# Kernel tuning notes

Hardware: AMD Instinct MI355X
Metric: run time of the kernel (lower is better)

Reference implementation:

```python
import jax, jax.numpy as jnp
import numpy as np


def _ln(x, g, b, eps=1e-5):
    m = x.mean(-1, keepdims=True)
    v = ((x - m) ** 2).mean(-1, keepdims=True)
    return (x - m) / jnp.sqrt(v + eps) * g + b


def _conv(x, w, b, stride, pad, groups):
    # x: NCHW, w: OIHW (I = in_ch/groups)
    out = jax.lax.conv_general_dilated(
        x, w, (stride, stride), [(pad, pad), (pad, pad)],
        dimension_numbers=('NCHW', 'OIHW', 'NCHW'), feature_group_count=groups)
    return out + b[None, :, None, None]


def _gelu(x):
    return jax.nn.gelu(x, approximate=False)  # torch nn.GELU (exact erf)


def _forward(x, H, W, lpu_w, lpu_b, n1_g, n1_b, conv2d_w, conv2d_b, cn_g, cn_b,
             q_w, sr1_w, sr1_b, an1_g, an1_b, sr2_w, sr2_b, an2_g, an2_b,
             kv1_w, kv2_w, proj_w, proj_b, n2_g, n2_b,
             fc1_w, fc1_b, dw_w, dw_b, fc2_w, fc2_b):
    B, N, C = x.shape
    cd = C // 4          # conv_part_dim = 64
    ad = C - cd          # attn_part_dim = 192
    nh = 8
    hg = nh // 2         # heads per group
    hd = ad // nh        # head_dim = 24
    scale = hd ** -0.5
    # ---- LPU: depthwise 3x3 conv residual ----
    xi = x.transpose(0, 2, 1).reshape(B, C, H, W)
    xi = _conv(xi, lpu_w, lpu_b, 1, 1, C) + xi
    x = xi.reshape(B, C, N).transpose(0, 2, 1)
    # ---- Attention branch (pre-LN) ----
    y = _ln(x, n1_g, n1_b)
    cp, ap = y[..., :cd], y[..., cd:]
    # conv part: dense 3x3 conv (sr_ratio==8 -> kernel 3, pad 1), then LN+GELU in NLC
    cp = cp.reshape(B, H, W, cd).transpose(0, 3, 1, 2)
    cp = _conv(cp, conv2d_w, conv2d_b, 1, 1, 1).reshape(B, cd, N).transpose(0, 2, 1)
    cp = _gelu(_ln(cp, cn_g, cn_b))
    # attn part: dual spatial-reduction KV paths
    q = (ap @ q_w.T).reshape(B, N, nh, hd).transpose(0, 2, 1, 3)  # [B,nh,N,hd]
    x_ = ap.transpose(0, 2, 1).reshape(B, ad, H, W)
    x1 = _conv(x_, sr1_w, sr1_b, 8, 0, ad).reshape(B, ad, -1).transpose(0, 2, 1)  # [B,(H/8)(W/8),ad]
    x1 = _gelu(_ln(x1, an1_g, an1_b))
    x2 = _conv(x_, sr2_w, sr2_b, 4, 0, ad).reshape(B, ad, -1).transpose(0, 2, 1)  # [B,(H/4)(W/4),ad]
    x2 = _gelu(_ln(x2, an2_g, an2_b))
    kv1 = (x1 @ kv1_w.T).reshape(B, -1, 2, hg, hd).transpose(2, 0, 3, 1, 4)  # [2,B,hg,M1,hd]
    kv2 = (x2 @ kv2_w.T).reshape(B, -1, 2, hg, hd).transpose(2, 0, 3, 1, 4)

    def attn(qh, k, v):
        a = jax.nn.softmax(jnp.einsum('bhnd,bhmd->bhnm', qh, k) * scale, axis=-1)
        o = jnp.einsum('bhnm,bhmd->bhnd', a, v)
        return o.transpose(0, 2, 1, 3).reshape(B, N, -1)

    o1 = attn(q[:, :hg], kv1[0], kv1[1])
    o2 = attn(q[:, hg:], kv2[0], kv2[1])
    y = jnp.concatenate([o1, o2, cp], axis=-1) @ proj_w.T + proj_b
    x = x + y
    # ---- MLP with depthwise conv ----
    z = _ln(x, n2_g, n2_b) @ fc1_w.T + fc1_b
    hidc = z.shape[-1]
    z = z.transpose(0, 2, 1).reshape(B, hidc, H, W)
    z = _conv(z, dw_w, dw_b, 1, 1, hidc).reshape(B, hidc, N).transpose(0, 2, 1)
    z = _gelu(z) @ fc2_w.T + fc2_b
    return x + z


def setup_inputs() -> dict:
    key = jax.random.key(0)
    ks = jax.random.split(key, 16)
    B, H, W, C = 16, 56, 56, 256
    N = H * W
    cd, ad = C // 4, C * 3 // 4
    hid = 4 * C
    f = lambda i, shape, s=0.02: jax.random.normal(ks[i], shape, jnp.float32) * s
    return dict(
        x=jax.random.normal(ks[0], (B, N, C), jnp.float32),
        H=H, W=W,
        lpu_w=f(1, (C, 1, 3, 3), 0.1), lpu_b=jnp.zeros((C,), jnp.float32),
        n1_g=jnp.ones((C,), jnp.float32), n1_b=jnp.zeros((C,), jnp.float32),
        conv2d_w=f(2, (cd, cd, 3, 3), 0.05), conv2d_b=jnp.zeros((cd,), jnp.float32),
        cn_g=jnp.ones((cd,), jnp.float32), cn_b=jnp.zeros((cd,), jnp.float32),
        q_w=f(3, (ad, ad)),
        sr1_w=f(4, (ad, 1, 8, 8), 0.1), sr1_b=jnp.zeros((ad,), jnp.float32),
        an1_g=jnp.ones((ad,), jnp.float32), an1_b=jnp.zeros((ad,), jnp.float32),
        sr2_w=f(5, (ad, 1, 4, 4), 0.1), sr2_b=jnp.zeros((ad,), jnp.float32),
        an2_g=jnp.ones((ad,), jnp.float32), an2_b=jnp.zeros((ad,), jnp.float32),
        kv1_w=f(6, (ad, ad)), kv2_w=f(7, (ad, ad)),
        proj_w=f(8, (C, C)), proj_b=jnp.zeros((C,), jnp.float32),
        n2_g=jnp.ones((C,), jnp.float32), n2_b=jnp.zeros((C,), jnp.float32),
        fc1_w=f(9, (hid, C)), fc1_b=jnp.zeros((hid,), jnp.float32),
        dw_w=f(10, (hid, 1, 3, 3), 0.1), dw_b=jnp.zeros((hid,), jnp.float32),
        fc2_w=f(11, (C, hid)), fc2_b=jnp.zeros((C,), jnp.float32),
    )


def reference(x, H, W, lpu_w, lpu_b, n1_g, n1_b, conv2d_w, conv2d_b, cn_g, cn_b,
              q_w, sr1_w, sr1_b, an1_g, an1_b, sr2_w, sr2_b, an2_g, an2_b,
              kv1_w, kv2_w, proj_w, proj_b, n2_g, n2_b,
              fc1_w, fc1_b, dw_w, dw_b, fc2_w, fc2_b):
    return _forward(x, H, W, lpu_w, lpu_b, n1_g, n1_b, conv2d_w, conv2d_b, cn_g, cn_b,
                    q_w, sr1_w, sr1_b, an1_g, an1_b, sr2_w, sr2_b, an2_g, an2_b,
                    kv1_w, kv2_w, proj_w, proj_b, n2_g, n2_b,
                    fc1_w, fc1_b, dw_w, dw_b, fc2_w, fc2_b)
```

## Files before the change

kernel.cpp:

```cpp
#include <hip/hip_runtime.h>
#include <math.h>

#define BB   16
#define HH   56
#define WW   56
#define NN   (HH*WW)
#define CC   256
#define CD   64
#define AD   192
#define NH   8
#define HG   4
#define HD   24
#define HID  1024
#define M1   49
#define M2   196
#define BNR  (BB*NN)

typedef __attribute__((ext_vector_type(8))) short s8v;
typedef __attribute__((ext_vector_type(4))) short s4v;
typedef __attribute__((ext_vector_type(4))) float f4v;
typedef __attribute__((ext_vector_type(8))) _Float16 h8v;
typedef __attribute__((ext_vector_type(2))) _Float16 h2v;

__device__ __forceinline__ float gelu_f(float x) {
    float u = x * (1.0f + 0.044715f * x * x);
    float t = __expf(-1.5957691216f * u);
    return x * __builtin_amdgcn_rcpf(1.0f + t);
}
__device__ __forceinline__ ushort f2bf(float f) {
    union { float f; uint32_t u; } c; c.f = f;
    uint32_t u = c.u;
    return (ushort)((u + 0x7fffu + ((u >> 16) & 1u)) >> 16);
}
__device__ __forceinline__ float bf2f(ushort u) {
    union { uint32_t u; float f; } c; c.u = ((uint32_t)u) << 16;
    return c.f;
}
__device__ __forceinline__ ushort f2h(float f) {
    union { _Float16 h; ushort u; } c; c.h = (_Float16)f;
    return c.u;
}
__device__ __forceinline__ void load_lds16(const void* gsrc, void* ldst) {
    __builtin_amdgcn_global_load_lds(
        (const __attribute__((address_space(1))) void*)gsrc,
        (__attribute__((address_space(3))) void*)ldst, 16, 0, 0);
}
__device__ __forceinline__ int xcd_swz(int bid, int nwg) {
    int q = nwg >> 3, r = nwg & 7;
    int x = bid & 7, i = bid >> 3;
    return (x < r ? x * (q + 1) : r * (q + 1) + (x - r) * q) + i;
}

__global__ __launch_bounds__(256) void wprep_kernel(
        const float* __restrict__ qw, const float* __restrict__ k1,
        const float* __restrict__ k2, const float* __restrict__ pw,
        const float* __restrict__ f1, const float* __restrict__ f2,
        const float* __restrict__ cw, const float* __restrict__ lw,
        const float* __restrict__ dw,
        ushort* __restrict__ wq, ushort* __restrict__ wkv1,
        ushort* __restrict__ wkv2, ushort* __restrict__ wpr,
        ushort* __restrict__ wf1, ushort* __restrict__ wf2,
        ushort* __restrict__ wcp, float* __restrict__ lpwt,
        ushort* __restrict__ dwwth) {
    int i = blockIdx.x * 256 + threadIdx.x;
    if (i < 36864) { wq[i] = f2bf(qw[i]); return; } i -= 36864;
    if (i < 36864) { wkv1[i] = f2bf(k1[i]); return; } i -= 36864;
    if (i < 36864) { wkv2[i] = f2bf(k2[i]); return; } i -= 36864;
    if (i < 65536) { wpr[i] = f2bf(pw[i]); return; } i -= 65536;
    if (i < 262144) { wf1[i] = f2bf(f1[i]); return; } i -= 262144;
    if (i < 262144) { wf2[i] = f2h(f2[i]); return; } i -= 262144;
    if (i < 36864) {
        int co = i / 576, k = i - co * 576;
        int tap = k >> 6, ci = k & 63;
        wcp[i] = f2bf(cw[co * 576 + ci * 9 + tap]);
        return;
    } i -= 36864;
    if (i < 2304) { int c = i / 9, t = i - c * 9; lpwt[t * CC + c] = lw[i]; return; } i -= 2304;
    if (i < 9216) { int c = i / 9, t = i - c * 9; dwwth[t * HID + c] = f2h(dw[i]); }
}

__global__ __launch_bounds__(256) void lpu_kernel(const float* __restrict__ x,
        const float* __restrict__ wt, const float* __restrict__ bias,
        const float* __restrict__ n1g, const float* __restrict__ n1b,
        ushort* __restrict__ xbuf, ushort* __restrict__ ybuf) {
    int tid = threadIdx.x;
    int lane = tid & 63, wv = tid >> 6;
    int c = lane * 4;
    int grp = xcd_swz(blockIdx.x, NN / 16) * 4 + wv;
    int n0 = grp * 4;
    int h = n0 / WW, x0 = n0 - h * WW;
    int b = blockIdx.y;
    const float* xb = x + (size_t)b * NN * CC + c;
    float4 wreg[9];
#pragma unroll
    for (int t = 0; t < 9; ++t) wreg[t] = *(const float4*)(wt + t * CC + c);
    float4 bz = *(const float4*)(bias + c);
    float4 acc[4] = {bz, bz, bz, bz};
#pragma unroll
    for (int cx = 0; cx < 6; ++cx) {
        int wx = x0 + cx - 1;
        if ((unsigned)wx >= (unsigned)WW) continue;
#pragma unroll
        for (int ky = 0; ky < 3; ++ky) {
            int hy = h + ky - 1;
            if ((unsigned)hy >= (unsigned)HH) continue;
            float4 xv = *(const float4*)(xb + (size_t)(hy * WW + wx) * CC);
#pragma unroll
            for (int xo = 0; xo < 4; ++xo) {
                int kx = cx - xo;
                if (kx < 0 || kx > 2) continue;
                float4 wv4 = wreg[ky * 3 + kx];
                acc[xo].x = fmaf(xv.x, wv4.x, acc[xo].x);
                acc[xo].y = fmaf(xv.y, wv4.y, acc[xo].y);
                acc[xo].z = fmaf(xv.z, wv4.z, acc[xo].z);
                acc[xo].w = fmaf(xv.w, wv4.w, acc[xo].w);
            }
        }
    }
    float4 gv = *(const float4*)(n1g + c);
    float4 bv = *(const float4*)(n1b + c);
#pragma unroll
    for (int xo = 0; xo < 4; ++xo) {
        size_t o = ((size_t)b * NN + n0 + xo) * CC + c;
        float4 rv = *(const float4*)(x + o);
        float4 a = acc[xo];
        a.x += rv.x; a.y += rv.y; a.z += rv.z; a.w += rv.w;
        s4v xv4;
        xv4.x = (short)f2bf(a.x);
        xv4.y = (short)f2bf(a.y);
        xv4.z = (short)f2bf(a.z);
        xv4.w = (short)f2bf(a.w);
        *(s4v*)(xbuf + o) = xv4;
        float s = a.x + a.y + a.z + a.w;
        float sq = a.x * a.x + a.y * a.y + a.z * a.z + a.w * a.w;
#pragma unroll
        for (int off = 32; off >= 1; off >>= 1) {
            s += __shfl_xor(s, off, 64);
            sq += __shfl_xor(sq, off, 64);
        }
        float mean = s * (1.0f / 256.0f);
        float var = sq * (1.0f / 256.0f) - mean * mean;
        float rstd = rsqrtf(var + 1e-5f);
        s4v ov;
        ov.x = (short)f2bf((a.x - mean) * rstd * gv.x + bv.x);
        ov.y = (short)f2bf((a.y - mean) * rstd * gv.y + bv.y);
        ov.z = (short)f2bf((a.z - mean) * rstd * gv.z + bv.z);
        ov.w = (short)f2bf((a.w - mean) * rstd * gv.w + bv.w);
        *(s4v*)(ybuf + o) = ov;
    }
}

__device__ __forceinline__ void cpgemm_body(
        const ushort* __restrict__ y, const ushort* __restrict__ wt,
        const float* __restrict__ cb, const float* __restrict__ cng,
        const float* __restrict__ cnb, ushort* __restrict__ cat,
        ushort* As , ushort* Ws , int tile) {
    int tid = threadIdx.x;
    int wid = tid >> 6, lane = tid & 63;
    int rt = xcd_swz(tile, BNR / 128) * 128;
    int r0 = tid >> 2, c0 = tid & 3;
    int r1 = r0 + 64;
    int tok0 = rt + r0, tok1 = rt + r1;
    int b0 = tok0 / NN, n0 = tok0 - b0 * NN, h0 = n0 / WW, w0 = n0 - h0 * WW;
    int b1 = tok1 / NN, n1 = tok1 - b1 * NN, h1 = n1 / WW, w1 = n1 - h1 * WW;
    const ushort* Wp = wt + (size_t)r0 * 576 + c0 * 8;
    int aw0 = (c0 ^ (r0 & 3)) << 3;
    f4v acc[2][4];
#pragma unroll
    for (int m = 0; m < 2; ++m)
#pragma unroll
        for (int n = 0; n < 4; ++n) acc[m][n] = (f4v)0.f;
    int lr = lane & 15, g4 = lane >> 4;
    int swz = (g4 ^ (lr & 3)) << 3;
    for (int kt = 0; kt < 576; kt += 32) {
        int tap = kt >> 6, ci0 = kt & 63;
        int t3 = tap / 3, dy = t3 - 1, dx = (tap - t3 * 3) - 1;
        s8v a0 = (s8v)0, a1 = (s8v)0;
        int hy0 = h0 + dy, wx0 = w0 + dx;
        if ((unsigned)hy0 < (unsigned)HH && (unsigned)wx0 < (unsigned)WW)
            a0 = *(const s8v*)(y + ((size_t)b0 * NN + hy0 * WW + wx0) * CC + ci0 + c0 * 8);
        int hy1 = h1 + dy, wx1 = w1 + dx;
        if ((unsigned)hy1 < (unsigned)HH && (unsigned)wx1 < (unsigned)WW)
            a1 = *(const s8v*)(y + ((size_t)b1 * NN + hy1 * WW + wx1) * CC + ci0 + c0 * 8);
        s8v wv = *(const s8v*)(Wp + kt);
        __syncthreads();
        *(s8v*)&As[r0 * 32 + aw0] = a0;
        *(s8v*)&As[r1 * 32 + aw0] = a1;
        *(s8v*)&Ws[r0 * 32 + aw0] = wv;
        __syncthreads();
        s8v af[2], bf[4];
#pragma unroll
        for (int m = 0; m < 2; ++m)
            af[m] = *(const s8v*)&As[(wid * 32 + m * 16 + lr) * 32 + swz];
#pragma unroll
        for (int n = 0; n < 4; ++n)
            bf[n] = *(const s8v*)&Ws[(n * 16 + lr) * 32 + swz];
#pragma unroll
        for (int m = 0; m < 2; ++m)
#pragma unroll
            for (int n = 0; n < 4; ++n)
                acc[m][n] = __builtin_amdgcn_mfma_f32_16x16x32_bf16(af[m], bf[n], acc[m][n], 0, 0, 0);
    }
    float gv[4], bv[4], cbv[4];
#pragma unroll
    for (int n = 0; n < 4; ++n) {
        int gc = n * 16 + lr;
        cbv[n] = cb[gc];
        gv[n] = cng[gc];
        bv[n] = cnb[gc];
    }
#pragma unroll
    for (int m = 0; m < 2; ++m)
#pragma unroll
        for (int r = 0; r < 4; ++r) {
            float s = 0.f, sq = 0.f;
#pragma unroll
            for (int n = 0; n < 4; ++n) {
                float v = acc[m][n][r] + cbv[n];
                acc[m][n][r] = v;
                s += v; sq += v * v;
            }
#pragma unroll
            for (int off = 1; off < 16; off <<= 1) {
                s += __shfl_xor(s, off, 64);
                sq += __shfl_xor(sq, off, 64);
            }
            float mean = s * (1.0f / 64.0f);
            float var = sq * (1.0f / 64.0f) - mean * mean;
            float rstd = rsqrtf(var + 1e-5f);
            int row = rt + wid * 32 + m * 16 + g4 * 4 + r;
            ushort* op = cat + (size_t)row * CC + 192;
#pragma unroll
            for (int n = 0; n < 4; ++n) {
                float v = (acc[m][n][r] - mean) * rstd * gv[n] + bv[n];
                op[n * 16 + lr] = f2bf(gelu_f(v));
            }
        }
}

template <int KS, int OW>
__device__ __forceinline__ void sr_body(const ushort* __restrict__ yap,
        const float* __restrict__ w, const float* __restrict__ bias,
        const float* __restrict__ g, const float* __restrict__ bt,
        ushort* __restrict__ out, int m, int b) {
    int ch = threadIdx.x;
    int oh = m / OW, ow = m - oh * OW;
    const ushort* yb = yap + (size_t)b * NN * CC;
    float acc = bias[ch];
#pragma unroll
    for (int ky = 0; ky < KS; ++ky)
#pragma unroll
        for (int kx = 0; kx < KS; ++kx)
            acc = fmaf(bf2f(yb[(size_t)((oh * KS + ky) * WW + ow * KS + kx) * CC + ch]),
                       w[ch * KS * KS + ky * KS + kx], acc);
    __shared__ float red[2][3];
    float s = acc, sq = acc * acc;
#pragma unroll
    for (int off = 32; off >= 1; off >>= 1) {
        s += __shfl_xor(s, off, 64);
        sq += __shfl_xor(sq, off, 64);
    }
    int wv = threadIdx.x >> 6, lane = threadIdx.x & 63;
    if (lane == 0) { red[0][wv] = s; red[1][wv] = sq; }
    __syncthreads();
    s = red[0][0] + red[0][1] + red[0][2];
    sq = red[1][0] + red[1][1] + red[1][2];
    float mean = s * (1.0f / 192.0f);
    float var = sq * (1.0f / 192.0f) - mean * mean;
    float rstd = rsqrtf(var + 1e-5f);
    float v = (acc - mean) * rstd * g[ch] + bt[ch];
    out[((size_t)b * (OW * OW) + m) * AD + ch] = f2bf(gelu_f(v));
}

__global__ __launch_bounds__(192) void sr_both(const ushort* __restrict__ yap,
        const float* __restrict__ w1, const float* __restrict__ b1,
        const float* __restrict__ g1, const float* __restrict__ t1,
        ushort* __restrict__ o1,
        const float* __restrict__ w2, const float* __restrict__ b2,
        const float* __restrict__ g2, const float* __restrict__ t2,
        ushort* __restrict__ o2) {
    int b = blockIdx.y;
    if (blockIdx.x < M2) sr_body<4, 14>(yap, w2, b2, g2, t2, o2, blockIdx.x, b);
    else                 sr_body<8, 7>(yap, w1, b1, g1, t1, o1, blockIdx.x - M2, b);
}

template <int MODE, int F16>
__device__ __forceinline__ void gemm_body(
        const ushort* __restrict__ A, int lda,
        const ushort* __restrict__ W, int K, int O,
        const float* __restrict__ bias,
        const ushort* __restrict__ res, int ldr,
        void* __restrict__ Cout, int ldc, int R,
        int gx, int nwg, int bid) {
    __shared__ __align__(16) ushort As[2 * 256 * 32];
    __shared__ __align__(16) ushort Ws[2 * 128 * 32];
    int tid = threadIdx.x;
    int w8 = tid >> 6, lane = tid & 63;
    int wr = w8 >> 1, wc = w8 & 1;
    int swzb = xcd_swz(bid, nwg);
    int rt = (swzb / gx) * 256, ot = (swzb % gx) * 128;
    int r0 = tid >> 2, cslot = tid & 3;
    int csrc = (cslot ^ (r0 & 3)) * 8;
    const ushort* Ap0 = A + (size_t)min(rt + r0, R - 1) * lda + csrc;
    const ushort* Ap1 = A + (size_t)min(rt + r0 + 128, R - 1) * lda + csrc;
    const ushort* Wp0 = W + (size_t)min(ot + r0, O - 1) * K + csrc;
    char* lA0 = (char*)As + w8 * 1024;
    char* lA1 = (char*)As + 8192 + w8 * 1024;
    char* lW0 = (char*)Ws + w8 * 1024;
    f4v acc[4][4];
#pragma unroll
    for (int m = 0; m < 4; ++m)
#pragma unroll
        for (int n = 0; n < 4; ++n) acc[m][n] = (f4v)0.f;
    int lr = lane & 15;
    int swz = ((lane >> 4) ^ (lr & 3)) << 3;
    load_lds16(Ap0, lA0);
    load_lds16(Ap1, lA1);
    load_lds16(Wp0, lW0);
    __syncthreads();
    int cur = 0;
    for (int kt = 0; kt < K; kt += 32) {
        if (kt + 32 < K) {
            int pa = (cur ^ 1) * 16384, pw = (cur ^ 1) * 8192;
            load_lds16(Ap0 + kt + 32, lA0 + pa);
            load_lds16(Ap1 + kt + 32, lA1 + pa);
            load_lds16(Wp0 + kt + 32, lW0 + pw);
        }
        const ushort* Ab = As + cur * 8192;
        const ushort* Wb = Ws + cur * 4096;
        s8v af[4], bf[4];
#pragma unroll
        for (int m = 0; m < 4; ++m)
            af[m] = *(const s8v*)&Ab[(wr * 64 + m * 16 + lr) * 32 + swz];
#pragma unroll
        for (int n = 0; n < 4; ++n)
            bf[n] = *(const s8v*)&Wb[(wc * 64 + n * 16 + lr) * 32 + swz];
#pragma unroll
        for (int m = 0; m < 4; ++m)
#pragma unroll
            for (int n = 0; n < 4; ++n) {
                if (F16) {
                    h8v ah = *(const h8v*)&af[m];
                    h8v bh = *(const h8v*)&bf[n];
                    acc[m][n] = __builtin_amdgcn_mfma_f32_16x16x32_f16(ah, bh, acc[m][n], 0, 0, 0);
                } else {
                    acc[m][n] = __builtin_amdgcn_mfma_f32_16x16x32_bf16(af[m], bf[n], acc[m][n], 0, 0, 0);
                }
            }
        __syncthreads();
        cur ^= 1;
    }
#pragma unroll
    for (int m = 0; m < 4; ++m)
#pragma unroll
        for (int n = 0; n < 4; ++n) {
            int gr = rt + wr * 64 + m * 16 + (lane >> 4) * 4;
            int gc = ot + wc * 64 + n * 16 + (lane & 15);
            if (gc >= O) continue;
#pragma unroll
            for (int r = 0; r < 4; ++r) {
                int row = gr + r;
                if (row >= R) continue;
                float v = acc[m][n][r];
                if (MODE & 1) v += bias[gc];
                if (MODE & 2) v += bf2f(res[(size_t)row * ldr + gc]);
                if (MODE & 4)      ((ushort*)Cout)[(size_t)row * ldc + gc] = f2bf(v);
                else if (MODE & 8) ((ushort*)Cout)[(size_t)row * ldc + gc] = f2h(v);
                else               ((float*)Cout)[(size_t)row * ldc + gc] = v;
            }
        }
}

__global__ __launch_bounds__(512) void kvq_all(
        const ushort* __restrict__ yap, const ushort* __restrict__ wq,
        ushort* __restrict__ qbuf,
        const ushort* __restrict__ x1g, const ushort* __restrict__ wkv1,
        ushort* __restrict__ kv1b,
        const ushort* __restrict__ x2g, const ushort* __restrict__ wkv2,
        ushort* __restrict__ kv2b) {
    int bid = blockIdx.y * 2 + blockIdx.x;
    if (blockIdx.z == 0) {
        gemm_body<4, 0>(yap, CC, wq, AD, AD, nullptr, nullptr, 0,
                        qbuf, AD, BNR, 2, 392, bid);
    } else if (blockIdx.z == 1) {
        if (blockIdx.y >= 4) return;
        gemm_body<4, 0>(x1g, AD, wkv1, AD, AD, nullptr, nullptr, 0,
                        kv1b, AD, BB * M1, 2, 8, bid);
    } else {
        if (blockIdx.y >= 13) return;
        gemm_body<4, 0>(x2g, AD, wkv2, AD, AD, nullptr, nullptr, 0,
                        kv2b, AD, BB * M2, 2, 26, bid);
    }
}

template <int MODE, int F16 = 0>
__global__ __launch_bounds__(512, 4) void gemm_8ph(
        const ushort* __restrict__ A, int lda,
        const ushort* __restrict__ W, int K, int O,
        const float* __restrict__ bias,
        const ushort* __restrict__ res, int ldr,
        void* __restrict__ Cout, int ldc, int R) {
    __shared__ __align__(16) ushort Al[2 * 128 * 32];
    __shared__ __align__(16) ushort Wl[2 * 256 * 32];
    int tid = threadIdx.x;
    int w8 = tid >> 6, lane = tid & 63;
    int wr = w8 >> 2, wc = w8 & 3;
    int nwg = gridDim.x * gridDim.y;
    int swzb = xcd_swz(blockIdx.y * gridDim.x + blockIdx.x, nwg);
    int rt = (swzb / gridDim.x) * 128, ot = (swzb % gridDim.x) * 256;
    int lr = lane & 15, g4 = lane >> 4;
    int swz = (g4 ^ (lr & 3)) << 3;
    int ar0 = tid >> 2, sp0 = tid & 3;
    int cs0 = ((sp0 ^ (ar0 & 3)) << 3);
    const ushort* Ap0 = A + (size_t)(rt + ar0) * lda + cs0;
    const ushort* Wp0 = W + (size_t)(ot + ar0) * K + cs0;
    const ushort* Wp1 = W + (size_t)(ot + ar0 + 128) * K + cs0;
    int d0 = w8 * 1024;
    f4v acc[4][4];
#pragma unroll
    for (int m = 0; m < 4; ++m)
#pragma unroll
        for (int n = 0; n < 4; ++n)
            acc[m][n] = (f4v)((MODE & 1) ? bias[ot + wc * 64 + n * 16 + lr] : 0.0f);
    auto STAGE = [&](int s) {
        int bo = s & 1;
        int kc = s * 32;
        load_lds16(Ap0 + kc, (char*)Al + bo * 8192 + d0);
        load_lds16(Wp0 + kc, (char*)Wl + bo * 16384 + d0);
        load_lds16(Wp1 + kc, (char*)Wl + bo * 16384 + 8192 + d0);
    };
    int nS = K >> 5;
    STAGE(0); STAGE(1);
    for (int s = 0; s < nS; ++s) {
        if (s == nS - 1) asm volatile("s_waitcnt vmcnt(0)" ::: "memory");
        else             asm volatile("s_waitcnt vmcnt(3)" ::: "memory");
        __builtin_amdgcn_s_barrier();
        __builtin_amdgcn_sched_barrier(0);
        const ushort* Ab = Al + (s & 1) * 4096;
        const ushort* Wb = Wl + (s & 1) * 8192;
        s8v af[4], bf[4];
#pragma unroll
        for (int m = 0; m < 4; ++m)
            af[m] = *(const s8v*)&Ab[(wr * 64 + m * 16 + lr) * 32 + swz];
#pragma unroll
        for (int n = 0; n < 4; ++n)
            bf[n] = *(const s8v*)&Wb[(wc * 64 + n * 16 + lr) * 32 + swz];
        __builtin_amdgcn_s_setprio(1);
#pragma unroll
        for (int m = 0; m < 4; ++m)
#pragma unroll
            for (int n = 0; n < 4; ++n) {
                if (F16) {
                    h8v ah = *(const h8v*)&af[m];
                    h8v bh = *(const h8v*)&bf[n];
                    acc[m][n] = __builtin_amdgcn_mfma_f32_16x16x32_f16(ah, bh, acc[m][n], 0, 0, 0);
                } else {
                    acc[m][n] = __builtin_amdgcn_mfma_f32_16x16x32_bf16(af[m], bf[n], acc[m][n], 0, 0, 0);
                }
            }
        __builtin_amdgcn_s_setprio(0);
        __builtin_amdgcn_s_barrier();
        if (s + 2 < nS) STAGE(s + 2);
    }
#pragma unroll
    for (int m = 0; m < 4; ++m) {
        int gr = rt + wr * 64 + m * 16 + g4 * 4;
#pragma unroll
        for (int n = 0; n < 4; ++n) {
            int gc = ot + wc * 64 + n * 16 + lr;
#pragma unroll
            for (int r = 0; r < 4; ++r) {
                int row = gr + r;
                float v = acc[m][n][r];
                if (MODE & 2) v += bf2f(res[(size_t)row * ldr + gc]);
                if (MODE & 4)      ((ushort*)Cout)[(size_t)row * ldc + gc] = f2bf(v);
                else if (MODE & 8) ((ushort*)Cout)[(size_t)row * ldc + gc] = f2h(v);
                else               ((float*)Cout)[(size_t)row * ldc + gc] = v;
            }
        }
    }
}

__global__ __launch_bounds__(512) void projln_kernel(
        const ushort* __restrict__ A, const ushort* __restrict__ W,
        const float* __restrict__ bias,
        const float* __restrict__ n2g, const float* __restrict__ n2b,
        ushort* __restrict__ xbuf, ushort* __restrict__ ybuf) {
    __shared__ __align__(16) ushort As[128 * 32];
    __shared__ __align__(16) ushort Ws[256 * 32];
    int tid = threadIdx.x;
    int w8 = tid >> 6, lane = tid & 63;
    int rt = xcd_swz(blockIdx.x, BNR / 128) * 128;
    int r0 = tid >> 2, cslot = tid & 3;
    int csrc = (cslot ^ (r0 & 3)) * 8;
    const ushort* Ap0 = A + (size_t)(rt + r0) * CC + csrc;
    const ushort* Wp0 = W + (size_t)r0 * CC + csrc;
    const ushort* Wp1 = W + (size_t)(r0 + 128) * CC + csrc;
    char* lA0 = (char*)As + w8 * 1024;
    char* lW0 = (char*)Ws + w8 * 1024;
    char* lW1 = (char*)Ws + 8192 + w8 * 1024;
    int lr = lane & 15, g4 = lane >> 4;
    int swz = (g4 ^ (lr & 3)) << 3;
    f4v acc[16];
#pragma unroll
    for (int n = 0; n < 16; ++n) acc[n] = (f4v)(bias[n * 16 + lr]);
    for (int kt = 0; kt < CC; kt += 32) {
        __syncthreads();
        load_lds16(Ap0 + kt, lA0);
        load_lds16(Wp0 + kt, lW0);
        load_lds16(Wp1 + kt, lW1);
        __syncthreads();
        s8v af = *(const s8v*)&As[(w8 * 16 + lr) * 32 + swz];
#pragma unroll
        for (int n = 0; n < 16; ++n) {
            s8v bf = *(const s8v*)&Ws[(n * 16 + lr) * 32 + swz];
            acc[n] = __builtin_amdgcn_mfma_f32_16x16x32_bf16(af, bf, acc[n], 0, 0, 0);
        }
    }
#pragma unroll
    for (int r = 0; r < 4; ++r) {
        int row = rt + w8 * 16 + g4 * 4 + r;
        ushort* xr = xbuf + (size_t)row * CC;
        ushort* yr = ybuf + (size_t)row * CC;
        float s = 0.f, sq = 0.f;
#pragma unroll
        for (int n = 0; n < 16; ++n) {
            float v = acc[n][r] + bf2f(xr[n * 16 + lr]);
            acc[n][r] = v;
            s += v; sq += v * v;
        }
#pragma unroll
        for (int off = 1; off < 16; off <<= 1) {
            s += __shfl_xor(s, off, 64);
            sq += __shfl_xor(sq, off, 64);
        }
        float mean = s * (1.0f / 256.0f);
        float var = sq * (1.0f / 256.0f) - mean * mean;
        float rstd = rsqrtf(var + 1e-5f);
#pragma unroll
        for (int n = 0; n < 16; ++n) {
            int col = n * 16 + lr;
            float v = acc[n][r];
            xr[col] = f2bf(v);
            yr[col] = f2bf((v - mean) * rstd * n2g[col] + n2b[col]);
        }
    }
}

template <int M, int MP>
__device__ __forceinline__ void attn_body(const ushort* __restrict__ q,
        const ushort* __restrict__ kvb, ushort* __restrict__ cat,
        ushort* Kl, ushort* VT, int g, int h, int b) {
    constexpr int NT = MP / 16;
    constexpr int NCH = MP / 32;
    int tid = threadIdx.x;
    for (int i = tid; i < MP * 4; i += 256) ((s8v*)Kl)[i] = (s8v)0;
    for (int i = tid; i < MP * 4; i += 256) ((s8v*)VT)[i] = (s8v)0;
    __syncthreads();
    for (int u = tid; u < M * 3; u += 256) {
        int m = u / 3, d0 = u - m * 3;
        s8v kv8 = *(const s8v*)(kvb + ((size_t)b * M + m) * AD + g * HD + d0 * 8);
        *(s8v*)&Kl[m * 32 + ((d0 ^ (m & 3)) << 3)] = kv8;
    }
    for (int u = tid; u < M * 3; u += 256) {
        int m = u / 3, d0 = u - m * 3;
        s8v vv = *(const s8v*)(kvb + ((size_t)b * M + m) * AD + 96 + g * HD + d0 * 8);
        int c = m >> 5, mm = m & 31;
        int gg = (mm >> 2) & 3;
        int t = (mm & 3) + ((mm & 16) >> 2);
#pragma unroll
        for (int j = 0; j < 8; ++j) {
            int d = d0 * 8 + j;
            VT[d * MP + ((c * 4 + (gg ^ (d & 3))) << 3) + t] = (ushort)vv[j];
        }
    }
    __syncthreads();
    int w = tid >> 6, lane = tid & 63;
    int ln = lane & 15, g4 = lane >> 4;
    int swz = (g4 ^ (ln & 3)) << 3;
    const float scale = 0.20412414523193154f;
    for (int nt = 0; nt < 4; ++nt) {
        int nbase = blockIdx.x * 256 + nt * 64;
        if (nbase >= NN) break;
        int n0 = nbase + w * 16 + ln;
        s8v qf = (s8v)0;
        if (g4 < 3) qf = *(const s8v*)(q + ((size_t)b * NN + n0) * AD + h * HD + g4 * 8);
        f4v sa[NT];
#pragma unroll
        for (int t = 0; t < NT; ++t) sa[t] = (f4v)0.f;
#pragma unroll
        for (int t = 0; t < NT; ++t) {
            s8v kf = *(const s8v*)&Kl[(t * 16 + ln) * 32 + swz];
            sa[t] = __builtin_amdgcn_mfma_f32_16x16x32_bf16(kf, qf, sa[t], 0, 0, 0);
        }
        float mx = -3.0e38f;
#pragma unroll
        for (int t = 0; t < NT; ++t)
#pragma unroll
            for (int r = 0; r < 4; ++r) {
                int m = t * 16 + g4 * 4 + r;
                float v = (m < M) ? sa[t][r] * scale : -3.0e38f;
                sa[t][r] = v;
                mx = fmaxf(mx, v);
            }
        mx = fmaxf(mx, __shfl_xor(mx, 16, 64));
        mx = fmaxf(mx, __shfl_xor(mx, 32, 64));
        float sum = 0.f;
#pragma unroll
        for (int t = 0; t < NT; ++t)
#pragma unroll
            for (int r = 0; r < 4; ++r) {
                float p = __expf(sa[t][r] - mx);
                sa[t][r] = p;
                sum += p;
            }
        sum += __shfl_xor(sum, 16, 64);
        sum += __shfl_xor(sum, 32, 64);
        float inv = 1.0f / sum;
        f4v oa[2] = {(f4v)0.f, (f4v)0.f};
#pragma unroll
        for (int c = 0; c < NCH; ++c) {
            s8v pb;
#pragma unroll
            for (int t = 0; t < 4; ++t) {
                pb[t]     = (short)f2bf(sa[c * 2][t]);
                pb[4 + t] = (short)f2bf(sa[c * 2 + 1][t]);
            }
#pragma unroll
            for (int dt = 0; dt < 2; ++dt) {
                s8v vf = *(const s8v*)&VT[(dt * 16 + ln) * MP + c * 32 + swz];
                oa[dt] = __builtin_amdgcn_mfma_f32_16x16x32_bf16(vf, pb, oa[dt], 0, 0, 0);
            }
        }
        ushort* op = cat + ((size_t)b * NN + n0) * CC + h * HD;
        s4v o0;
#pragma unroll
        for (int r = 0; r < 4; ++r) o0[r] = (short)f2bf(oa[0][r] * inv);
        *(s4v*)(op + g4 * 4) = o0;
        if (g4 < 2) {
            s4v o1;
#pragma unroll
            for (int r = 0; r < 4; ++r) o1[r] = (short)f2bf(oa[1][r] * inv);
            *(s4v*)(op + 16 + g4 * 4) = o1;
        }
    }
}

__global__ __launch_bounds__(256) void attn_both(const ushort* __restrict__ q,
        const ushort* __restrict__ kv1b, const ushort* __restrict__ kv2b,
        ushort* __restrict__ cat,
        const ushort* __restrict__ ybuf, const ushort* __restrict__ wcp,
        const float* __restrict__ cb, const float* __restrict__ cng,
        const float* __restrict__ cnb) {
    __shared__ __align__(16) ushort Kl[224 * 32];
    __shared__ __align__(16) ushort VT[32 * 224];
    int hy = blockIdx.y, b = blockIdx.z;
    if (hy < HG)      attn_body<M1, 64>(q, kv1b, cat, Kl, VT, hy, hy, b);
    else if (hy < NH) attn_body<M2, 224>(q, kv2b, cat, Kl, VT, hy - HG, hy, b);
    else {
        int id = blockIdx.x + 13 * blockIdx.z;
        for (int t = id * 2; t < id * 2 + 2; ++t)
            if (t < BNR / 128)
                cpgemm_body(ybuf, wcp, cb, cng, cnb, cat, Kl, VT, t);
    }
}

__global__ __launch_bounds__(256) void dwconv_kernel(const ushort* __restrict__ z1,
        const ushort* __restrict__ wt, const float* __restrict__ bias,
        ushort* __restrict__ z2) {
    int bid = xcd_swz(blockIdx.x, HH * 7);
    int h = bid / 7, bx = bid - h * 7;
    int b = blockIdx.y;
    int c = (threadIdx.x & 127) * 8;
    int x0 = bx * 8 + (threadIdx.x >> 7) * 4;
    const ushort* zrow = z1 + ((size_t)b * NN + h * WW) * HID + c;
    h2v wreg[9][4];
#pragma unroll
    for (int t = 0; t < 9; ++t) {
        s8v w8 = *(const s8v*)(wt + t * HID + c);
        const h2v* wp = (const h2v*)&w8;
#pragma unroll
        for (int p = 0; p < 4; ++p) wreg[t][p] = wp[p];
    }
    h2v acc[4][4];
    {
        float4 b0 = *(const float4*)(bias + c);
        float4 b1 = *(const float4*)(bias + c + 4);
        h2v bz[4];
        bz[0][0] = (_Float16)b0.x; bz[0][1] = (_Float16)b0.y;
        bz[1][0] = (_Float16)b0.z; bz[1][1] = (_Float16)b0.w;
        bz[2][0] = (_Float16)b1.x; bz[2][1] = (_Float16)b1.y;
        bz[3][0] = (_Float16)b1.z; bz[3][1] = (_Float16)b1.w;
#pragma unroll
        for (int xo = 0; xo < 4; ++xo)
#pragma unroll
            for (int p = 0; p < 4; ++p) acc[xo][p] = bz[p];
    }
#pragma unroll
    for (int cx = 0; cx < 6; ++cx) {
        int wx = x0 + cx - 1;
        if ((unsigned)wx >= (unsigned)WW) continue;
#pragma unroll
        for (int ky = 0; ky < 3; ++ky) {
            int hy = h + ky - 1;
            if ((unsigned)hy >= (unsigned)HH) continue;
            s8v v = *(const s8v*)(zrow + ((size_t)(ky - 1) * WW + wx) * HID);
            const h2v* v2 = (const h2v*)&v;
#pragma unroll
            for (int xo = 0; xo < 4; ++xo) {
                int kx = cx - xo;
                if (kx < 0 || kx > 2) continue;
#pragma unroll
                for (int p = 0; p < 4; ++p)
                    acc[xo][p] = v2[p] * wreg[ky * 3 + kx][p] + acc[xo][p];
            }
        }
    }
    ushort* zo = z2 + ((size_t)b * NN + h * WW + x0) * HID + c;
#pragma unroll
    for (int xo = 0; xo < 4; ++xo) {
        s8v o;
#pragma unroll
        for (int p = 0; p < 4; ++p) {
            o[p * 2]     = (short)f2h(gelu_f((float)acc[xo][p][0]));
            o[p * 2 + 1] = (short)f2h(gelu_f((float)acc[xo][p][1]));
        }
        *(s8v*)(zo + (size_t)xo * HID) = o;
    }
}

extern "C" void kernel_launch(void* const* d_in, const int* in_sizes, int n_in,
                              void* d_out, int out_size, void* d_ws, size_t ws_size,
                              hipStream_t stream) {
    const float* x      = (const float*)d_in[0];
    const float* lpu_w  = (const float*)d_in[3];
    const float* lpu_b  = (const float*)d_in[4];
    const float* n1_g   = (const float*)d_in[5];
    const float* n1_b   = (const float*)d_in[6];
    const float* c2_w   = (const float*)d_in[7];
    const float* c2_b   = (const float*)d_in[8];
    const float* cn_g   = (const float*)d_in[9];
    const float* cn_b   = (const float*)d_in[10];
    const float* q_w    = (const float*)d_in[11];
    const float* sr1_w  = (const float*)d_in[12];
    const float* sr1_b  = (const float*)d_in[13];
    const float* an1_g  = (const float*)d_in[14];
    const float* an1_b  = (const float*)d_in[15];
    const float* sr2_w  = (const float*)d_in[16];
    const float* sr2_b  = (const float*)d_in[17];
    const float* an2_g  = (const float*)d_in[18];
    const float* an2_b  = (const float*)d_in[19];
    const float* kv1_w  = (const float*)d_in[20];
    const float* kv2_w  = (const float*)d_in[21];
    const float* proj_w = (const float*)d_in[22];
    const float* proj_b = (const float*)d_in[23];
    const float* n2_g   = (const float*)d_in[24];
    const float* n2_b   = (const float*)d_in[25];
    const float* fc1_w  = (const float*)d_in[26];
    const float* fc1_b  = (const float*)d_in[27];
    const float* dw_w   = (const float*)d_in[28];
    const float* dw_b   = (const float*)d_in[29];
    const float* fc2_w  = (const float*)d_in[30];
    const float* fc2_b  = (const float*)d_in[31];
    float* out = (float*)d_out;

    char* ws = (char*)d_ws;
    size_t off = 0;
    auto allocB = [&](size_t bytes) {
        char* p = ws + off;
        off += ((bytes + 255) & ~(size_t)255);
        return p;
    };
    ushort* xbuf = (ushort*)allocB((size_t)BNR * CC * 2);
    ushort* ybuf = (ushort*)allocB((size_t)BNR * CC * 2);
    ushort* wq   = (ushort*)allocB((size_t)AD * AD * 2);
    ushort* wkv1 = (ushort*)allocB((size_t)AD * AD * 2);
    ushort* wkv2 = (ushort*)allocB((size_t)AD * AD * 2);
    ushort* wpr  = (ushort*)allocB((size_t)CC * CC * 2);
    ushort* wf1  = (ushort*)allocB((size_t)HID * CC * 2);
    ushort* wf2  = (ushort*)allocB((size_t)CC * HID * 2);
    ushort* wcp  = (ushort*)allocB((size_t)64 * 576 * 2);
    float*  lpwt = (float*)allocB((size_t)9 * CC * 4);
    ushort* dwwt = (ushort*)allocB((size_t)9 * HID * 2);
    size_t zmark = off;
    ushort* cat  = (ushort*)allocB((size_t)BNR * CC * 2);
    ushort* qbuf = (ushort*)allocB((size_t)BNR * AD * 2);
    ushort* x1g  = (ushort*)allocB((size_t)BB * M1 * AD * 2);
    ushort* x2g  = (ushort*)allocB((size_t)BB * M2 * AD * 2);
    ushort* kv1b = (ushort*)allocB((size_t)BB * M1 * AD * 2);
    ushort* kv2b = (ushort*)allocB((size_t)BB * M2 * AD * 2);

    int CB2 = 1;
    for (int cb = 16; cb >= 1; cb >>= 1) {
        if (zmark + 2 * (size_t)cb * NN * HID * 2 <= ws_size) { CB2 = cb; break; }
    }

    dim3 b256(256), b512(512);
    wprep_kernel<<<dim3(2925), b256, 0, stream>>>(
        q_w, kv1_w, kv2_w, proj_w, fc1_w, fc2_w, c2_w, lpu_w, dw_w,
        wq, wkv1, wkv2, wpr, wf1, wf2, wcp, lpwt, dwwt);
    lpu_kernel<<<dim3(NN / 16, BB), b256, 0, stream>>>(x, lpwt, lpu_b, n1_g, n1_b, xbuf, ybuf);
    sr_both<<<dim3(M1 + M2, BB), dim3(192), 0, stream>>>(ybuf + CD,
        sr1_w, sr1_b, an1_g, an1_b, x1g, sr2_w, sr2_b, an2_g, an2_b, x2g);
    kvq_all<<<dim3(2, 196, 3), b512, 0, stream>>>(
        ybuf + CD, wq, qbuf, x1g, wkv1, kv1b, x2g, wkv2, kv2b);
    attn_both<<<dim3((NN + 255) / 256, NH + 1, BB), b256, 0, stream>>>(
        qbuf, kv1b, kv2b, cat, ybuf, wcp, c2_b, cn_g, cn_b);
    projln_kernel<<<dim3(BNR / 128), b512, 0, stream>>>(
        cat, wpr, proj_b, n2_g, n2_b, xbuf, ybuf);
    ushort* z1 = (ushort*)(ws + zmark);
    ushort* z2 = z1 + (size_t)CB2 * NN * HID;
    for (int c0 = 0; c0 < BB; c0 += CB2) {
        size_t tokoff = (size_t)c0 * NN;
        int Rr = CB2 * NN;
        gemm_8ph<9><<<dim3(HID / 256, Rr / 128), b512, 0, stream>>>(
            ybuf + tokoff * CC, CC, wf1, CC, HID, fc1_b, nullptr, 0, z1, HID, Rr);
        dwconv_kernel<<<dim3(HH * 7, CB2), b256, 0, stream>>>(z1, dwwt, dw_b, z2);
        gemm_8ph<3, 1><<<dim3(CC / 256, Rr / 128), b512, 0, stream>>>(
            z2, HID, wf2, HID, CC, fc2_b, xbuf + tokoff * CC, CC, out + tokoff * CC, CC, Rr);
    }
}
```

Baseline: 333.3 us.

## Write V pre-transposed from KV GEMM and read K/V directly in attention

The KV projection epilogue now scatters V into a zero-initialised global buffer already in the MFMA-friendly transposed, swizzled order. The attention kernel then reads K and V fragments straight from global memory instead of staging them through LDS with zero-fill and two barriers. This removes per-block LDS staging work and shrinks shared memory in the attention kernel, which could raise occupancy. The trade-offs are strided global K loads, 2-byte scattered stores in the GEMM epilogue, and two extra memsets. Padded K rows now read neighbouring-batch data rather than zeros, so correctness relies on masking of keys beyond M.

```diff
diff --git a/kernel.cpp b/kernel.cpp
--- a/kernel.cpp
+++ b/kernel.cpp
@@ -284,14 +284,14 @@
     else                 sr_body<8, 7>(yap, w1, b1, g1, t1, o1, blockIdx.x - M2, b);
 }
 
-template <int MODE, int F16>
+template <int MODE, int F16, int MT = 0, int MPAD = 0>
 __device__ __forceinline__ void gemm_body(
         const ushort* __restrict__ A, int lda,
         const ushort* __restrict__ W, int K, int O,
         const float* __restrict__ bias,
         const ushort* __restrict__ res, int ldr,
         void* __restrict__ Cout, int ldc, int R,
-        int gx, int nwg, int bid) {
+        int gx, int nwg, int bid, ushort* __restrict__ vtb = nullptr) {
     __shared__ __align__(16) ushort As[2 * 256 * 32];
     __shared__ __align__(16) ushort Ws[2 * 128 * 32];
     int tid = threadIdx.x;
@@ -364,9 +364,16 @@
                 float v = acc[m][n][r];
                 if (MODE & 1) v += bias[gc];
                 if (MODE & 2) v += bf2f(res[(size_t)row * ldr + gc]);
-                if (MODE & 4)      ((ushort*)Cout)[(size_t)row * ldc + gc] = f2bf(v);
-                else if (MODE & 8) ((ushort*)Cout)[(size_t)row * ldc + gc] = f2h(v);
-                else               ((float*)Cout)[(size_t)row * ldc + gc] = v;
+                if (MT > 0 && gc >= 96) {
+                    int gg = (gc - 96) / HD, d = (gc - 96) - gg * HD;
+                    int bb = row / MT, mloc = row - bb * MT;
+                    int mm = mloc & 31;
+                    int idx = (mloc >> 5) * 32 + ((mm >> 2) & 3) * 8 + ((mm >> 4) & 1) * 4 + (mm & 3);
+                    vtb[(((size_t)bb * HG + gg) * HD + d) * MPAD + idx] = f2bf(v);
+                }
+                else if (MODE & 4)  ((ushort*)Cout)[(size_t)row * ldc + gc] = f2bf(v);
+                else if (MODE & 8)  ((ushort*)Cout)[(size_t)row * ldc + gc] = f2h(v);
+                else                ((float*)Cout)[(size_t)row * ldc + gc] = v;
             }
         }
 }
@@ -375,21 +382,21 @@
         const ushort* __restrict__ yap, const ushort* __restrict__ wq,
         ushort* __restrict__ qbuf,
         const ushort* __restrict__ x1g, const ushort* __restrict__ wkv1,
-        ushort* __restrict__ kv1b,
+        ushort* __restrict__ kv1b, ushort* __restrict__ vtb1,
         const ushort* __restrict__ x2g, const ushort* __restrict__ wkv2,
-        ushort* __restrict__ kv2b) {
+        ushort* __restrict__ kv2b, ushort* __restrict__ vtb2) {
     int bid = blockIdx.y * 2 + blockIdx.x;
     if (blockIdx.z == 0) {
         gemm_body<4, 0>(yap, CC, wq, AD, AD, nullptr, nullptr, 0,
                         qbuf, AD, BNR, 2, 392, bid);
     } else if (blockIdx.z == 1) {
         if (blockIdx.y >= 4) return;
-        gemm_body<4, 0>(x1g, AD, wkv1, AD, AD, nullptr, nullptr, 0,
-                        kv1b, AD, BB * M1, 2, 8, bid);
+        gemm_body<4, 0, M1, 64>(x1g, AD, wkv1, AD, AD, nullptr, nullptr, 0,
+                        kv1b, AD, BB * M1, 2, 8, bid, vtb1);
     } else {
         if (blockIdx.y >= 13) return;
-        gemm_body<4, 0>(x2g, AD, wkv2, AD, AD, nullptr, nullptr, 0,
-                        kv2b, AD, BB * M2, 2, 26, bid);
+        gemm_body<4, 0, M2, 224>(x2g, AD, wkv2, AD, AD, nullptr, nullptr, 0,
+                        kv2b, AD, BB * M2, 2, 26, bid, vtb2);
     }
 }
 
@@ -547,37 +554,17 @@
     }
 }
 
-template <int M, int MP>
+template <int M, int MP, int MPAD>
 __device__ __forceinline__ void attn_body(const ushort* __restrict__ q,
-        const ushort* __restrict__ kvb, ushort* __restrict__ cat,
-        ushort* Kl, ushort* VT, int g, int h, int b) {
+        const ushort* __restrict__ kvb, const ushort* __restrict__ vtb,
+        ushort* __restrict__ cat, int g, int h, int b) {
     constexpr int NT = MP / 16;
     constexpr int NCH = MP / 32;
     int tid = threadIdx.x;
-    for (int i = tid; i < MP * 4; i += 256) ((s8v*)Kl)[i] = (s8v)0;
-    for (int i = tid; i < MP * 4; i += 256) ((s8v*)VT)[i] = (s8v)0;
-    __syncthreads();
-    for (int u = tid; u < M * 3; u += 256) {
-        int m = u / 3, d0 = u - m * 3;
-        s8v kv8 = *(const s8v*)(kvb + ((size_t)b * M + m) * AD + g * HD + d0 * 8);
-        *(s8v*)&Kl[m * 32 + ((d0 ^ (m & 3)) << 3)] = kv8;
-    }
-    for (int u = tid; u < M * 3; u += 256) {
-        int m = u / 3, d0 = u - m * 3;
-        s8v vv = *(const s8v*)(kvb + ((size_t)b * M + m) * AD + 96 + g * HD + d0 * 8);
-        int c = m >> 5, mm = m & 31;
-        int gg = (mm >> 2) & 3;
-        int t = (mm & 3) + ((mm & 16) >> 2);
-#pragma unroll
-        for (int j = 0; j < 8; ++j) {
-            int d = d0 * 8 + j;
-            VT[d * MP + ((c * 4 + (gg ^ (d & 3))) << 3) + t] = (ushort)vv[j];
-        }
-    }
-    __syncthreads();
     int w = tid >> 6, lane = tid & 63;
     int ln = lane & 15, g4 = lane >> 4;
-    int swz = (g4 ^ (ln & 3)) << 3;
+    const ushort* kb = kvb + (size_t)b * M * AD + g * HD;
+    const ushort* vb = vtb + ((size_t)b * HG + g) * HD * MPAD;
     const float scale = 0.20412414523193154f;
     for (int nt = 0; nt < 4; ++nt) {
         int nbase = blockIdx.x * 256 + nt * 64;
@@ -590,7 +577,8 @@
         for (int t = 0; t < NT; ++t) sa[t] = (f4v)0.f;
 #pragma unroll
         for (int t = 0; t < NT; ++t) {
-            s8v kf = *(const s8v*)&Kl[(t * 16 + ln) * 32 + swz];
+            s8v kf = (s8v)0;
+            if (g4 < 3) kf = *(const s8v*)(kb + (size_t)(t * 16 + ln) * AD + g4 * 8);
             sa[t] = __builtin_amdgcn_mfma_f32_16x16x32_bf16(kf, qf, sa[t], 0, 0, 0);
         }
         float mx = -3.0e38f;
@@ -628,7 +616,9 @@
             }
 #pragma unroll
             for (int dt = 0; dt < 2; ++dt) {
-                s8v vf = *(const s8v*)&VT[(dt * 16 + ln) * MP + c * 32 + swz];
+                int d = dt * 16 + ln;
+                s8v vf = (s8v)0;
+                if (d < HD) vf = *(const s8v*)(vb + (size_t)d * MPAD + c * 32 + g4 * 8);
                 oa[dt] = __builtin_amdgcn_mfma_f32_16x16x32_bf16(vf, pb, oa[dt], 0, 0, 0);
             }
         }
@@ -647,21 +637,22 @@
 }
 
 __global__ __launch_bounds__(256) void attn_both(const ushort* __restrict__ q,
-        const ushort* __restrict__ kv1b, const ushort* __restrict__ kv2b,
+        const ushort* __restrict__ kv1b, const ushort* __restrict__ vtb1,
+        const ushort* __restrict__ kv2b, const ushort* __restrict__ vtb2,
         ushort* __restrict__ cat,
         const ushort* __restrict__ ybuf, const ushort* __restrict__ wcp,
         const float* __restrict__ cb, const float* __restrict__ cng,
         const float* __restrict__ cnb) {
-    __shared__ __align__(16) ushort Kl[224 * 32];
-    __shared__ __align__(16) ushort VT[32 * 224];
+    __shared__ __align__(16) ushort As[128 * 32];
+    __shared__ __align__(16) ushort Ws[64 * 32];
     int hy = blockIdx.y, b = blockIdx.z;
-    if (hy < HG)      attn_body<M1, 64>(q, kv1b, cat, Kl, VT, hy, hy, b);
-    else if (hy < NH) attn_body<M2, 224>(q, kv2b, cat, Kl, VT, hy - HG, hy, b);
+    if (hy < HG)      attn_body<M1, 64, 64>(q, kv1b, vtb1, cat, hy, hy, b);
+    else if (hy < NH) attn_body<M2, 224, 224>(q, kv2b, vtb2, cat, hy - HG, hy, b);
     else {
         int id = blockIdx.x + 13 * blockIdx.z;
         for (int t = id * 2; t < id * 2 + 2; ++t)
             if (t < BNR / 128)
-                cpgemm_body(ybuf, wcp, cb, cng, cnb, cat, Kl, VT, t);
+                cpgemm_body(ybuf, wcp, cb, cng, cnb, cat, As, Ws, t);
     }
 }
 
@@ -787,8 +778,10 @@
     ushort* qbuf = (ushort*)allocB((size_t)BNR * AD * 2);
     ushort* x1g  = (ushort*)allocB((size_t)BB * M1 * AD * 2);
     ushort* x2g  = (ushort*)allocB((size_t)BB * M2 * AD * 2);
-    ushort* kv1b = (ushort*)allocB((size_t)BB * M1 * AD * 2);
-    ushort* kv2b = (ushort*)allocB((size_t)BB * M2 * AD * 2);
+    ushort* kv1b = (ushort*)allocB(((size_t)BB * M1 + 64) * AD * 2);
+    ushort* kv2b = (ushort*)allocB(((size_t)BB * M2 + 64) * AD * 2);
+    ushort* vtb1 = (ushort*)allocB((size_t)BB * HG * HD * 64 * 2);
+    ushort* vtb2 = (ushort*)allocB((size_t)BB * HG * HD * 224 * 2);
 
     int CB2 = 1;
     for (int cb = 16; cb >= 1; cb >>= 1) {
@@ -796,6 +789,8 @@
     }
 
     dim3 b256(256), b512(512);
+    hipMemsetAsync(vtb1, 0, (size_t)BB * HG * HD * 64 * 2, stream);
+    hipMemsetAsync(vtb2, 0, (size_t)BB * HG * HD * 224 * 2, stream);
     wprep_kernel<<<dim3(2925), b256, 0, stream>>>(
         q_w, kv1_w, kv2_w, proj_w, fc1_w, fc2_w, c2_w, lpu_w, dw_w,
         wq, wkv1, wkv2, wpr, wf1, wf2, wcp, lpwt, dwwt);
@@ -803,9 +798,9 @@
     sr_both<<<dim3(M1 + M2, BB), dim3(192), 0, stream>>>(ybuf + CD,
         sr1_w, sr1_b, an1_g, an1_b, x1g, sr2_w, sr2_b, an2_g, an2_b, x2g);
     kvq_all<<<dim3(2, 196, 3), b512, 0, stream>>>(
-        ybuf + CD, wq, qbuf, x1g, wkv1, kv1b, x2g, wkv2, kv2b);
+        ybuf + CD, wq, qbuf, x1g, wkv1, kv1b, vtb1, x2g, wkv2, kv2b, vtb2);
     attn_both<<<dim3((NN + 255) / 256, NH + 1, BB), b256, 0, stream>>>(
-        qbuf, kv1b, kv2b, cat, ybuf, wcp, c2_b, cn_g, cn_b);
+        qbuf, kv1b, vtb1, kv2b, vtb2, cat, ybuf, wcp, c2_b, cn_g, cn_b);
     projln_kernel<<<dim3(BNR / 128), b512, 0, stream>>>(
         cat, wpr, proj_b, n2_g, n2_b, xbuf, ybuf);
     ushort* z1 = (ushort*)(ws + zmark);
```

Result: slower. 370.9 us (+11.3%).
